# Performance work log

Hardware: AMD Instinct MI355X
Metric: run time of the kernel (lower is better)

The kernel has to match this reference:

```python
import jax, jax.numpy as jnp
import numpy as np

ALPHA_MIN = float(np.exp(-1.0 / 5.0))   # balance=False lower clamp
ALPHA_MAX = float(np.exp(-1.0 / 25.0))  # balance=False upper clamp


@jax.custom_vjp
def spike(u, thr):
    # Heaviside forward: spike if membrane potential exceeds threshold
    return (u > thr).astype(u.dtype)

def _spike_fwd(u, thr):
    return spike(u, thr), (u, thr)

def _spike_bwd(res, g):
    u, thr = res
    # Boxcar surrogate gradient: pass-through within +-0.5 of threshold
    mask = ((u > thr - 0.5) & (u <= thr + 0.5)).astype(g.dtype)
    return (g * mask, jnp.zeros_like(thr))

spike.defvjp(_spike_fwd, _spike_bwd)


def setup_inputs() -> dict:
    key = jax.random.key(0)
    kx, kw, kv, ka = jax.random.split(key, 4)
    B, T, I, H = 32, 1000, 256, 512
    x = jax.random.normal(kx, (B, T, I), dtype=jnp.float32)
    # W ~ U(-sqrt(1/I), sqrt(1/I)) as in nn.init.uniform_
    lim = float(np.sqrt(1.0 / I))
    W = jax.random.uniform(kw, (H, I), minval=-lim, maxval=lim, dtype=jnp.float32)
    # V: orthogonal init
    V = jnp.linalg.qr(jax.random.normal(kv, (H, H), dtype=jnp.float32))[0]
    alpha = jax.random.uniform(ka, (H,), minval=ALPHA_MIN, maxval=ALPHA_MAX, dtype=jnp.float32)
    v_thresh = jnp.ones((H,), dtype=jnp.float32)
    return {"x": x, "W": W, "V": V, "alpha": alpha, "v_thresh": v_thresh}


def reference(x, W, V, alpha, v_thresh):
    # x: [B, T, I]; W: [H, I]; V: [H, H]; alpha, v_thresh: [H]
    a = jnp.clip(alpha, ALPHA_MIN, ALPHA_MAX)
    H = V.shape[0]
    Vz = V * (1.0 - jnp.eye(H, dtype=V.dtype))  # fill_diagonal_(0)
    Wx = jnp.einsum('bti,hi->bth', x, W)        # feedforward drive [B,T,H]

    B = x.shape[0]
    ut0 = jnp.zeros((B, H), dtype=x.dtype)
    st0 = jnp.zeros((B, H), dtype=x.dtype)

    def step(carry, wx_t):
        ut, st = carry
        # leaky integration with recurrent spikes (fix_w_rec=False path)
        ut = a * (ut - st) + (1.0 - a) * (wx_t + st @ Vz)
        st = spike(ut, v_thresh)
        return (ut, st), st

    _, s = jax.lax.scan(step, (ut0, st0), jnp.swapaxes(Wx, 0, 1))  # [T,B,H]
    return jnp.swapaxes(s, 0, 1)  # [B,T,H]
```

## Files before the change

### kernel.cpp

```cpp
#include <hip/hip_runtime.h>

#define BATCH 32
#define TSTEPS 1000
#define KDIM 256
#define HDIM 512
#define NSEG 8
#define SEGL 125
#define SPFD 25

#define ALPHA_MIN_F 0.8187307530779818f
#define ALPHA_MAX_F 0.9607894391523232f

typedef __attribute__((ext_vector_type(8))) short bf16x8;
typedef __attribute__((ext_vector_type(8))) unsigned short u16x8;
typedef __attribute__((ext_vector_type(4))) float f32x4;

static __device__ __forceinline__ unsigned short f2bf(float f) {
  unsigned u = __float_as_uint(f);
  u += 0x7FFF + ((u >> 16) & 1);
  return (unsigned short)(u >> 16);
}
static __device__ __forceinline__ float bf2f(unsigned short s) {
  return __uint_as_float(((unsigned)s) << 16);
}

__global__ void init_fs(int* fs) {
  if (threadIdx.x < BATCH) fs[threadIdx.x] = TSTEPS;
}

__global__ __launch_bounds__(256) void cast_pack(const float* __restrict__ src,
                                                 unsigned short* __restrict__ hi,
                                                 unsigned short* __restrict__ lo,
                                                 int ntiles) {
  const int tile = blockIdx.x * 4 + (threadIdx.x >> 6);
  if (tile >= ntiles) return;
  const int lane = threadIdx.x & 63;
  const int row = tile * 16 + (lane & 15);
  const int kg = lane >> 4;
  const float* sp = src + (size_t)row * KDIM + kg * 8;
  unsigned short* hp = hi + (size_t)tile * 8 * 512 + lane * 8;
  unsigned short* lp = lo + (size_t)tile * 8 * 512 + lane * 8;
#pragma unroll
  for (int ks = 0; ks < 8; ++ks) {
    float4 a = *reinterpret_cast<const float4*>(sp + ks * 32);
    float4 b = *reinterpret_cast<const float4*>(sp + ks * 32 + 4);
    u16x8 h, l;
    h[0] = f2bf(a.x); l[0] = f2bf(a.x - bf2f(h[0]));
    h[1] = f2bf(a.y); l[1] = f2bf(a.y - bf2f(h[1]));
    h[2] = f2bf(a.z); l[2] = f2bf(a.z - bf2f(h[2]));
    h[3] = f2bf(a.w); l[3] = f2bf(a.w - bf2f(h[3]));
    h[4] = f2bf(b.x); l[4] = f2bf(b.x - bf2f(h[4]));
    h[5] = f2bf(b.y); l[5] = f2bf(b.y - bf2f(h[5]));
    h[6] = f2bf(b.z); l[6] = f2bf(b.z - bf2f(h[6]));
    h[7] = f2bf(b.w); l[7] = f2bf(b.w - bf2f(h[7]));
    *reinterpret_cast<u16x8*>(hp + ks * 512) = h;
    *reinterpret_cast<u16x8*>(lp + ks * 512) = l;
  }
}

__global__ __launch_bounds__(128, 2) void gemm_mfma3(
    const float* __restrict__ x, const unsigned short* __restrict__ wph,
    const unsigned short* __restrict__ wpl, float* __restrict__ wx) {
  __shared__ short bsh[2][2][4096];
  const int tid = threadIdx.x;
  const int lane = tid & 63;
  const int wid = tid >> 6;
  const int row = lane & 15;
  const int kg = lane >> 4;
  const int tm = blockIdx.x * 2 + wid;
  const int m0 = tm * 16;

  bf16x8 ah[8], al[8];
  const float* xp = x + (size_t)(m0 + row) * KDIM + kg * 8;
#pragma unroll
  for (int ks = 0; ks < 8; ++ks) {
    float4 f0 = *reinterpret_cast<const float4*>(xp + ks * 32);
    float4 f1 = *reinterpret_cast<const float4*>(xp + ks * 32 + 4);
    bf16x8 hv, lv;
    hv[0] = (short)f2bf(f0.x); lv[0] = (short)f2bf(f0.x - bf2f(hv[0]));
    hv[1] = (short)f2bf(f0.y); lv[1] = (short)f2bf(f0.y - bf2f(hv[1]));
    hv[2] = (short)f2bf(f0.z); lv[2] = (short)f2bf(f0.z - bf2f(hv[2]));
    hv[3] = (short)f2bf(f0.w); lv[3] = (short)f2bf(f0.w - bf2f(hv[3]));
    hv[4] = (short)f2bf(f1.x); lv[4] = (short)f2bf(f1.x - bf2f(hv[4]));
    hv[5] = (short)f2bf(f1.y); lv[5] = (short)f2bf(f1.y - bf2f(hv[5]));
    hv[6] = (short)f2bf(f1.z); lv[6] = (short)f2bf(f1.z - bf2f(hv[6]));
    hv[7] = (short)f2bf(f1.w); lv[7] = (short)f2bf(f1.w - bf2f(hv[7]));
    ah[ks] = hv;
    al[ks] = lv;
  }

#pragma unroll
  for (int r = 0; r < 4; ++r) {
    const int o = r * 1024 + tid * 8;
    *reinterpret_cast<bf16x8*>(&bsh[0][0][o]) =
        *reinterpret_cast<const bf16x8*>(wph + o);
    *reinterpret_cast<bf16x8*>(&bsh[0][1][o]) =
        *reinterpret_cast<const bf16x8*>(wpl + o);
  }
  __syncthreads();

  for (int ct = 0; ct < 32; ++ct) {
    const int buf = ct & 1;
    bf16x8 nh[4], nl[4];
    const bool pre = (ct < 31);
    if (pre) {
      const unsigned short* sh = wph + (size_t)(ct + 1) * 4096;
      const unsigned short* sl = wpl + (size_t)(ct + 1) * 4096;
#pragma unroll
      for (int r = 0; r < 4; ++r) {
        const int o = r * 1024 + tid * 8;
        nh[r] = *reinterpret_cast<const bf16x8*>(sh + o);
        nl[r] = *reinterpret_cast<const bf16x8*>(sl + o);
      }
    }

    f32x4 accA = {0.f, 0.f, 0.f, 0.f};
    f32x4 accB = {0.f, 0.f, 0.f, 0.f};
    f32x4 accC = {0.f, 0.f, 0.f, 0.f};
#pragma unroll
    for (int ks = 0; ks < 8; ++ks) {
      bf16x8 bh = *reinterpret_cast<const bf16x8*>(&bsh[buf][0][ks * 512 + lane * 8]);
      bf16x8 bl = *reinterpret_cast<const bf16x8*>(&bsh[buf][1][ks * 512 + lane * 8]);
      accA = __builtin_amdgcn_mfma_f32_16x16x32_bf16(ah[ks], bh, accA, 0, 0, 0);
      accB = __builtin_amdgcn_mfma_f32_16x16x32_bf16(al[ks], bh, accB, 0, 0, 0);
      accC = __builtin_amdgcn_mfma_f32_16x16x32_bf16(ah[ks], bl, accC, 0, 0, 0);
    }
    const int n0 = ct * 16;
#pragma unroll
    for (int j = 0; j < 4; ++j) {
      wx[(size_t)(m0 + kg * 4 + j) * HDIM + n0 + row] =
          (accA[j] + accB[j]) + accC[j];
    }
    if (pre) {
#pragma unroll
      for (int r = 0; r < 4; ++r) {
        const int o = r * 1024 + tid * 8;
        *reinterpret_cast<bf16x8*>(&bsh[buf ^ 1][0][o]) = nh[r];
        *reinterpret_cast<bf16x8*>(&bsh[buf ^ 1][1][o]) = nl[r];
      }
    }
    __syncthreads();
  }
}

__global__ __launch_bounds__(64) void seg_sum(const float* __restrict__ wx,
                                              const float* __restrict__ alpha,
                                              float* __restrict__ cbuf) {
  const int hb = blockIdx.x & 7;
  const int rest = blockIdx.x >> 3;
  const int seg = rest % 7;
  const int b = rest / 7;
  const int h = (hb << 6) + threadIdx.x;
  const float a = fminf(fmaxf(alpha[h], ALPHA_MIN_F), ALPHA_MAX_F);
  const float na = 1.0f - a;
  const float* wp = wx + ((size_t)b * TSTEPS + seg * SEGL) * HDIM + h;

  float pf[SPFD];
#pragma unroll
  for (int d = 0; d < SPFD; ++d) pf[d] = wp[(size_t)d * HDIM];

  float c = 0.f;
  for (int j0 = 0; j0 < SEGL; j0 += SPFD) {
#pragma unroll
    for (int js = 0; js < SPFD; ++js) {
      const int j = j0 + js;
      const float w = pf[js];
      int jp = j + SPFD;
      if (jp > SEGL - 1) jp = SEGL - 1;
      pf[js] = wp[(size_t)jp * HDIM];
      c = fmaf(a, c, na * w);
    }
  }
  cbuf[(size_t)seg * BATCH * HDIM + (size_t)b * HDIM + h] = c;
}

__global__ __launch_bounds__(64) void seg_scan(const float* __restrict__ wx,
                                               const float* __restrict__ alpha,
                                               const float* __restrict__ vthr,
                                               const float* __restrict__ cbuf,
                                               float* __restrict__ out,
                                               int* __restrict__ fs) {
  const int hb = blockIdx.x & 7;
  const int seg = (blockIdx.x >> 3) & 7;
  const int b = blockIdx.x >> 6;
  const int h = (hb << 6) + threadIdx.x;
  const float a = fminf(fmaxf(alpha[h], ALPHA_MIN_F), ALPHA_MAX_F);
  const float na = 1.0f - a;
  const float th = vthr[h];
  const int t0g = seg * SEGL;
  const float* wp = wx + ((size_t)b * TSTEPS + t0g) * HDIM + h;
  float* op = out + ((size_t)b * TSTEPS + t0g) * HDIM + h;

  float pf[SPFD];
#pragma unroll
  for (int d = 0; d < SPFD; ++d) pf[d] = wp[(size_t)d * HDIM];

  float aL = 1.0f;
  for (int i = 0; i < SEGL; ++i) aL *= a;
  float u = 0.f;
  for (int k = 0; k < seg; ++k)
    u = fmaf(aL, u, cbuf[(size_t)k * BATCH * HDIM + (size_t)b * HDIM + h]);

  float s = 0.f;
  int first = TSTEPS;
  for (int j0 = 0; j0 < SEGL; j0 += SPFD) {
#pragma unroll
    for (int js = 0; js < SPFD; ++js) {
      const int j = j0 + js;
      const float w = pf[js];
      int jp = j + SPFD;
      if (jp > SEGL - 1) jp = SEGL - 1;
      pf[js] = wp[(size_t)jp * HDIM];
      u = fmaf(a, u - s, na * w);
      s = (u > th) ? 1.0f : 0.0f;
      op[(size_t)j * HDIM] = s;
      if (s != 0.0f && first == TSTEPS) {
        first = t0g + j;
        atomicMin(&fs[b], first);
      }
    }
  }
}

static __device__ __forceinline__ void scan_body(const float* wxbuf,
                                                 const float* __restrict__ V,
                                                 const float* __restrict__ alpha,
                                                 const float* __restrict__ vthr,
                                                 float* out, int b) {
  const int l = threadIdx.x;
  const int h0 = 4 * l;
  const int h1 = 256 + 4 * l;

  float4 al0 = *reinterpret_cast<const float4*>(alpha + h0);
  float4 al1 = *reinterpret_cast<const float4*>(alpha + h1);
  float4 th0 = *reinterpret_cast<const float4*>(vthr + h0);
  float4 th1 = *reinterpret_cast<const float4*>(vthr + h1);
  float a[8] = {al0.x, al0.y, al0.z, al0.w, al1.x, al1.y, al1.z, al1.w};
  float th[8] = {th0.x, th0.y, th0.z, th0.w, th1.x, th1.y, th1.z, th1.w};
  float na[8], u[8], s[8], r[8];
#pragma unroll
  for (int j = 0; j < 8; ++j) {
    float c = fminf(fmaxf(a[j], ALPHA_MIN_F), ALPHA_MAX_F);
    a[j] = c; na[j] = 1.0f - c;
    u[j] = 0.f; s[j] = 0.f; r[j] = 0.f;
  }
  const float* wb = wxbuf + (size_t)b * TSTEPS * HDIM;
  float* ob = out + (size_t)b * TSTEPS * HDIM;
  float4 p0[4], p1[4];
#pragma unroll
  for (int d = 0; d < 4; ++d) {
    p0[d] = *reinterpret_cast<const float4*>(wb + (size_t)d * HDIM + h0);
    p1[d] = *reinterpret_cast<const float4*>(wb + (size_t)d * HDIM + h1);
  }
  for (int t0 = 0; t0 < TSTEPS; t0 += 4) {
#pragma unroll
    for (int ts = 0; ts < 4; ++ts) {
      const int t = t0 + ts;
      float w8[8] = {p0[ts].x, p0[ts].y, p0[ts].z, p0[ts].w,
                     p1[ts].x, p1[ts].y, p1[ts].z, p1[ts].w};
      int tpre = t + 4;
      if (tpre > TSTEPS - 1) tpre = TSTEPS - 1;
      p0[ts] = *reinterpret_cast<const float4*>(wb + (size_t)tpre * HDIM + h0);
      p1[ts] = *reinterpret_cast<const float4*>(wb + (size_t)tpre * HDIM + h1);
#pragma unroll
      for (int j = 0; j < 8; ++j) {
        float un = fmaf(a[j], u[j] - s[j], na[j] * (w8[j] + r[j]));
        u[j] = un;
        s[j] = (un > th[j]) ? 1.0f : 0.0f;
      }
      *reinterpret_cast<float4*>(ob + (size_t)t * HDIM + h0) =
          make_float4(s[0], s[1], s[2], s[3]);
      *reinterpret_cast<float4*>(ob + (size_t)t * HDIM + h1) =
          make_float4(s[4], s[5], s[6], s[7]);
      float ssum = s[0] + s[1] + s[2] + s[3] + s[4] + s[5] + s[6] + s[7];
      unsigned long long anym = __ballot(ssum != 0.0f);
      if (anym != 0ull) {
        unsigned long long mk[8];
#pragma unroll
        for (int j = 0; j < 8; ++j) mk[j] = __ballot(s[j] != 0.0f);
        float rr[8] = {0.f, 0.f, 0.f, 0.f, 0.f, 0.f, 0.f, 0.f};
#pragma unroll
        for (int j2 = 0; j2 < 8; ++j2) {
          unsigned long long m = mk[j2];
          while (m) {
            int src = __builtin_ctzll(m);
            m &= m - 1;
            int hin = (j2 < 4) ? (src * 4 + j2) : (256 + src * 4 + (j2 - 4));
            const float* vrow = V + (size_t)hin * HDIM;
            float4 v0 = *reinterpret_cast<const float4*>(vrow + h0);
            float4 v1 = *reinterpret_cast<const float4*>(vrow + h1);
            float vv[8] = {v0.x, v0.y, v0.z, v0.w, v1.x, v1.y, v1.z, v1.w};
#pragma unroll
            for (int j = 0; j < 8; ++j) {
              int hj = (j < 4) ? (h0 + j) : (h1 + j - 4);
              rr[j] += (hj == hin) ? 0.0f : vv[j];
            }
          }
        }
#pragma unroll
        for (int j = 0; j < 8; ++j) r[j] = rr[j];
      } else {
#pragma unroll
        for (int j = 0; j < 8; ++j) r[j] = 0.0f;
      }
    }
  }
}

__global__ __launch_bounds__(64) void fallback_scan(
    const float* wxbuf, const float* __restrict__ V,
    const float* __restrict__ alpha, const float* __restrict__ vthr,
    float* out, const int* __restrict__ fs) {
  const int b = blockIdx.x;
  if (fs[b] >= TSTEPS - 1) return;
  scan_body(wxbuf, V, alpha, vthr, out, b);
}

__global__ __launch_bounds__(64) void rlif_scan(const float* wxbuf,
                                                const float* __restrict__ V,
                                                const float* __restrict__ alpha,
                                                const float* __restrict__ vthr,
                                                float* out) {
  scan_body(wxbuf, V, alpha, vthr, out, blockIdx.x);
}

__global__ __launch_bounds__(256) void gemm_xwT(const float* __restrict__ x,
                                                const float* __restrict__ W,
                                                float* __restrict__ wx) {
  __shared__ float As[32][64];
  __shared__ float Bs[32][64];
  const int m0 = blockIdx.x * 64;
  const int n0 = blockIdx.y * 64;
  const int tid = threadIdx.x;
  const int tx = tid & 15;
  const int ty = tid >> 4;
  const int lr = tid >> 2;
  const int lk = (tid & 3) * 8;

  float acc[4][4] = {};
  for (int k0 = 0; k0 < KDIM; k0 += 32) {
    const float4* ap =
        reinterpret_cast<const float4*>(x + (size_t)(m0 + lr) * KDIM + k0 + lk);
    const float4* bp =
        reinterpret_cast<const float4*>(W + (size_t)(n0 + lr) * KDIM + k0 + lk);
    float4 a0 = ap[0], a1 = ap[1];
    float4 b0 = bp[0], b1 = bp[1];
    __syncthreads();
    As[lk + 0][lr] = a0.x; As[lk + 1][lr] = a0.y;
    As[lk + 2][lr] = a0.z; As[lk + 3][lr] = a0.w;
    As[lk + 4][lr] = a1.x; As[lk + 5][lr] = a1.y;
    As[lk + 6][lr] = a1.z; As[lk + 7][lr] = a1.w;
    Bs[lk + 0][lr] = b0.x; Bs[lk + 1][lr] = b0.y;
    Bs[lk + 2][lr] = b0.z; Bs[lk + 3][lr] = b0.w;
    Bs[lk + 4][lr] = b1.x; Bs[lk + 5][lr] = b1.y;
    Bs[lk + 6][lr] = b1.z; Bs[lk + 7][lr] = b1.w;
    __syncthreads();
#pragma unroll
    for (int k = 0; k < 32; ++k) {
      float4 av = *reinterpret_cast<const float4*>(&As[k][ty * 4]);
      float4 bv = *reinterpret_cast<const float4*>(&Bs[k][tx * 4]);
      float am[4] = {av.x, av.y, av.z, av.w};
      float bn[4] = {bv.x, bv.y, bv.z, bv.w};
#pragma unroll
      for (int i = 0; i < 4; ++i)
#pragma unroll
        for (int j = 0; j < 4; ++j) acc[i][j] = fmaf(am[i], bn[j], acc[i][j]);
    }
  }
#pragma unroll
  for (int i = 0; i < 4; ++i) {
    float4 o = make_float4(acc[i][0], acc[i][1], acc[i][2], acc[i][3]);
    *reinterpret_cast<float4*>(wx + (size_t)(m0 + ty * 4 + i) * HDIM + n0 +
                               tx * 4) = o;
  }
}

extern "C" void kernel_launch(void* const* d_in, const int* in_sizes, int n_in,
                              void* d_out, int out_size, void* d_ws,
                              size_t ws_size, hipStream_t stream) {
  const float* x = (const float*)d_in[0];
  const float* W = (const float*)d_in[1];
  const float* V = (const float*)d_in[2];
  const float* alpha = (const float*)d_in[3];
  const float* vthr = (const float*)d_in[4];
  float* out = (float*)d_out;

  const size_t wx_b = (size_t)BATCH * TSTEPS * HDIM * 4;
  const size_t wh_b = (size_t)HDIM * KDIM * 2;
  const size_t cb_b = (size_t)NSEG * BATCH * HDIM * 4;
  const size_t needA = wx_b + 2 * wh_b + cb_b + 128;
  const size_t needB = wx_b + cb_b + 128;

  char* ws = (char*)d_ws;
  if (ws_size >= needA) {
    float* wx = (float*)ws;
    unsigned short* wph = (unsigned short*)(ws + wx_b);
    unsigned short* wpl = wph + (size_t)HDIM * KDIM;
    float* cbuf = (float*)(ws + wx_b + 2 * wh_b);
    int* fs = (int*)(ws + wx_b + 2 * wh_b + cb_b);

    hipLaunchKernelGGL(init_fs, dim3(1), dim3(64), 0, stream, fs);
    hipLaunchKernelGGL(cast_pack, dim3(8), dim3(256), 0, stream, W, wph, wpl,
                       HDIM / 16);
    hipLaunchKernelGGL(gemm_mfma3, dim3(BATCH * TSTEPS / 32), dim3(128), 0,
                       stream, x, wph, wpl, wx);
    hipLaunchKernelGGL(seg_sum, dim3(BATCH * 7 * 8), dim3(64), 0, stream,
                       wx, alpha, cbuf);
    hipLaunchKernelGGL(seg_scan, dim3(BATCH * NSEG * 8), dim3(64), 0, stream,
                       wx, alpha, vthr, cbuf, out, fs);
    hipLaunchKernelGGL(fallback_scan, dim3(BATCH), dim3(64), 0, stream, wx, V,
                       alpha, vthr, out, fs);
  } else if (ws_size >= needB) {
    float* wx = (float*)ws;
    float* cbuf = (float*)(ws + wx_b);
    int* fs = (int*)(ws + wx_b + cb_b);
    hipLaunchKernelGGL(init_fs, dim3(1), dim3(64), 0, stream, fs);
    hipLaunchKernelGGL(gemm_xwT, dim3(BATCH * TSTEPS / 64, HDIM / 64),
                       dim3(256), 0, stream, x, W, wx);
    hipLaunchKernelGGL(seg_sum, dim3(BATCH * 7 * 8), dim3(64), 0, stream,
                       wx, alpha, cbuf);
    hipLaunchKernelGGL(seg_scan, dim3(BATCH * NSEG * 8), dim3(64), 0, stream,
                       wx, alpha, vthr, cbuf, out, fs);
    hipLaunchKernelGGL(fallback_scan, dim3(BATCH), dim3(64), 0, stream, wx, V,
                       alpha, vthr, out, fs);
  } else {
    float* wx = (ws_size >= wx_b) ? (float*)ws : out;
    hipLaunchKernelGGL(gemm_xwT, dim3(BATCH * TSTEPS / 64, HDIM / 64),
                       dim3(256), 0, stream, x, W, wx);
    hipLaunchKernelGGL(rlif_scan, dim3(BATCH), dim3(64), 0, stream, wx, V,
                       alpha, vthr, out);
  }
}
```

Baseline: 82.65 us.

## Compute two M-tiles per wave in split-bf16 GEMM and fold fs init into cast kernel

Each wave in the MFMA GEMM now processes two 16-row M tiles, so every B fragment read from shared memory is reused twice and the grid is halved. Separately, the fs initialisation moves into the weight cast kernel, removing one kernel launch. The larger tile doubles the A-fragment and accumulator registers per wave, which can lower occupancy, and halving the block count reduces parallelism across CUs.

```diff
diff --git a/kernel.cpp b/kernel.cpp
--- a/kernel.cpp
+++ b/kernel.cpp
@@ -28,10 +28,10 @@
   if (threadIdx.x < BATCH) fs[threadIdx.x] = TSTEPS;
 }
 
-__global__ __launch_bounds__(256) void cast_pack(const float* __restrict__ src,
-                                                 unsigned short* __restrict__ hi,
-                                                 unsigned short* __restrict__ lo,
-                                                 int ntiles) {
+__global__ __launch_bounds__(256) void cast_pack_fs(
+    const float* __restrict__ src, unsigned short* __restrict__ hi,
+    unsigned short* __restrict__ lo, int ntiles, int* __restrict__ fs) {
+  if (blockIdx.x == 0 && threadIdx.x < BATCH) fs[threadIdx.x] = TSTEPS;
   const int tile = blockIdx.x * 4 + (threadIdx.x >> 6);
   if (tile >= ntiles) return;
   const int lane = threadIdx.x & 63;
@@ -58,7 +58,7 @@
   }
 }
 
-__global__ __launch_bounds__(128, 2) void gemm_mfma3(
+__global__ __launch_bounds__(128, 2) void gemm_mfma7(
     const float* __restrict__ x, const unsigned short* __restrict__ wph,
     const unsigned short* __restrict__ wpl, float* __restrict__ wx) {
   __shared__ short bsh[2][2][4096];
@@ -67,26 +67,28 @@
   const int wid = tid >> 6;
   const int row = lane & 15;
   const int kg = lane >> 4;
-  const int tm = blockIdx.x * 2 + wid;
-  const int m0 = tm * 16;
-
-  bf16x8 ah[8], al[8];
-  const float* xp = x + (size_t)(m0 + row) * KDIM + kg * 8;
-#pragma unroll
-  for (int ks = 0; ks < 8; ++ks) {
-    float4 f0 = *reinterpret_cast<const float4*>(xp + ks * 32);
-    float4 f1 = *reinterpret_cast<const float4*>(xp + ks * 32 + 4);
-    bf16x8 hv, lv;
-    hv[0] = (short)f2bf(f0.x); lv[0] = (short)f2bf(f0.x - bf2f(hv[0]));
-    hv[1] = (short)f2bf(f0.y); lv[1] = (short)f2bf(f0.y - bf2f(hv[1]));
-    hv[2] = (short)f2bf(f0.z); lv[2] = (short)f2bf(f0.z - bf2f(hv[2]));
-    hv[3] = (short)f2bf(f0.w); lv[3] = (short)f2bf(f0.w - bf2f(hv[3]));
-    hv[4] = (short)f2bf(f1.x); lv[4] = (short)f2bf(f1.x - bf2f(hv[4]));
-    hv[5] = (short)f2bf(f1.y); lv[5] = (short)f2bf(f1.y - bf2f(hv[5]));
-    hv[6] = (short)f2bf(f1.z); lv[6] = (short)f2bf(f1.z - bf2f(hv[6]));
-    hv[7] = (short)f2bf(f1.w); lv[7] = (short)f2bf(f1.w - bf2f(hv[7]));
-    ah[ks] = hv;
-    al[ks] = lv;
+  const int tmb = (blockIdx.x * 2 + wid) * 2;
+
+  bf16x8 ah[2][8], al[2][8];
+#pragma unroll
+  for (int mt = 0; mt < 2; ++mt) {
+    const float* xp = x + (size_t)((tmb + mt) * 16 + row) * KDIM + kg * 8;
+#pragma unroll
+    for (int ks = 0; ks < 8; ++ks) {
+      float4 f0 = *reinterpret_cast<const float4*>(xp + ks * 32);
+      float4 f1 = *reinterpret_cast<const float4*>(xp + ks * 32 + 4);
+      bf16x8 hv, lv;
+      hv[0] = (short)f2bf(f0.x); lv[0] = (short)f2bf(f0.x - bf2f(hv[0]));
+      hv[1] = (short)f2bf(f0.y); lv[1] = (short)f2bf(f0.y - bf2f(hv[1]));
+      hv[2] = (short)f2bf(f0.z); lv[2] = (short)f2bf(f0.z - bf2f(hv[2]));
+      hv[3] = (short)f2bf(f0.w); lv[3] = (short)f2bf(f0.w - bf2f(hv[3]));
+      hv[4] = (short)f2bf(f1.x); lv[4] = (short)f2bf(f1.x - bf2f(hv[4]));
+      hv[5] = (short)f2bf(f1.y); lv[5] = (short)f2bf(f1.y - bf2f(hv[5]));
+      hv[6] = (short)f2bf(f1.z); lv[6] = (short)f2bf(f1.z - bf2f(hv[6]));
+      hv[7] = (short)f2bf(f1.w); lv[7] = (short)f2bf(f1.w - bf2f(hv[7]));
+      ah[mt][ks] = hv;
+      al[mt][ks] = lv;
+    }
   }
 
 #pragma unroll
@@ -114,22 +116,29 @@
       }
     }
 
-    f32x4 accA = {0.f, 0.f, 0.f, 0.f};
-    f32x4 accB = {0.f, 0.f, 0.f, 0.f};
-    f32x4 accC = {0.f, 0.f, 0.f, 0.f};
+    f32x4 accA[2] = {{0.f, 0.f, 0.f, 0.f}, {0.f, 0.f, 0.f, 0.f}};
+    f32x4 accB[2] = {{0.f, 0.f, 0.f, 0.f}, {0.f, 0.f, 0.f, 0.f}};
+    f32x4 accC[2] = {{0.f, 0.f, 0.f, 0.f}, {0.f, 0.f, 0.f, 0.f}};
 #pragma unroll
     for (int ks = 0; ks < 8; ++ks) {
       bf16x8 bh = *reinterpret_cast<const bf16x8*>(&bsh[buf][0][ks * 512 + lane * 8]);
       bf16x8 bl = *reinterpret_cast<const bf16x8*>(&bsh[buf][1][ks * 512 + lane * 8]);
-      accA = __builtin_amdgcn_mfma_f32_16x16x32_bf16(ah[ks], bh, accA, 0, 0, 0);
-      accB = __builtin_amdgcn_mfma_f32_16x16x32_bf16(al[ks], bh, accB, 0, 0, 0);
-      accC = __builtin_amdgcn_mfma_f32_16x16x32_bf16(ah[ks], bl, accC, 0, 0, 0);
+#pragma unroll
+      for (int mt = 0; mt < 2; ++mt) {
+        accA[mt] = __builtin_amdgcn_mfma_f32_16x16x32_bf16(ah[mt][ks], bh, accA[mt], 0, 0, 0);
+        accB[mt] = __builtin_amdgcn_mfma_f32_16x16x32_bf16(al[mt][ks], bh, accB[mt], 0, 0, 0);
+        accC[mt] = __builtin_amdgcn_mfma_f32_16x16x32_bf16(ah[mt][ks], bl, accC[mt], 0, 0, 0);
+      }
     }
     const int n0 = ct * 16;
 #pragma unroll
-    for (int j = 0; j < 4; ++j) {
-      wx[(size_t)(m0 + kg * 4 + j) * HDIM + n0 + row] =
-          (accA[j] + accB[j]) + accC[j];
+    for (int mt = 0; mt < 2; ++mt) {
+      const int m0 = (tmb + mt) * 16;
+#pragma unroll
+      for (int j = 0; j < 4; ++j) {
+        wx[(size_t)(m0 + kg * 4 + j) * HDIM + n0 + row] =
+            (accA[mt][j] + accB[mt][j]) + accC[mt][j];
+      }
     }
     if (pre) {
 #pragma unroll
@@ -399,10 +408,9 @@
     float* cbuf = (float*)(ws + wx_b + 2 * wh_b);
     int* fs = (int*)(ws + wx_b + 2 * wh_b + cb_b);
 
-    hipLaunchKernelGGL(init_fs, dim3(1), dim3(64), 0, stream, fs);
-    hipLaunchKernelGGL(cast_pack, dim3(8), dim3(256), 0, stream, W, wph, wpl,
-                       HDIM / 16);
-    hipLaunchKernelGGL(gemm_mfma3, dim3(BATCH * TSTEPS / 32), dim3(128), 0,
+    hipLaunchKernelGGL(cast_pack_fs, dim3(8), dim3(256), 0, stream, W, wph,
+                       wpl, HDIM / 16, fs);
+    hipLaunchKernelGGL(gemm_mfma7, dim3(BATCH * TSTEPS / 64), dim3(128), 0,
                        stream, x, wph, wpl, wx);
     hipLaunchKernelGGL(seg_sum, dim3(BATCH * 7 * 8), dim3(64), 0, stream,
                        wx, alpha, cbuf);
```

Measured after the change: 88.76 us. 7.4% more time.

## Fuse segment sum and segment scan into one cooperative kernel with grid sync

Applied to the files above, without the earlier changes.

Replaces the separate seg_sum and seg_scan kernels with a single cooperative kernel. Each block loads its 125-step segment of wx into registers once, computes the segment carry, waits at a grid-wide sync, then runs the spike scan from the register copy. This removes the second read of wx from global memory and one kernel launch. init_fs is also folded into cast_pack to drop another launch. The trade-offs are a 125-float register array per thread, which may spill, and the requirement that all 2048 blocks be co-resident for the grid sync.

```diff
diff --git a/kernel.cpp b/kernel.cpp
--- a/kernel.cpp
+++ b/kernel.cpp
@@ -1,4 +1,7 @@
 #include <hip/hip_runtime.h>
+#include <hip/hip_cooperative_groups.h>
+
+namespace cg = cooperative_groups;
 
 #define BATCH 32
 #define TSTEPS 1000
@@ -28,10 +31,10 @@
   if (threadIdx.x < BATCH) fs[threadIdx.x] = TSTEPS;
 }
 
-__global__ __launch_bounds__(256) void cast_pack(const float* __restrict__ src,
-                                                 unsigned short* __restrict__ hi,
-                                                 unsigned short* __restrict__ lo,
-                                                 int ntiles) {
+__global__ __launch_bounds__(256) void cast_pack_fs(
+    const float* __restrict__ src, unsigned short* __restrict__ hi,
+    unsigned short* __restrict__ lo, int ntiles, int* __restrict__ fs) {
+  if (blockIdx.x == 0 && threadIdx.x < BATCH) fs[threadIdx.x] = TSTEPS;
   const int tile = blockIdx.x * 4 + (threadIdx.x >> 6);
   if (tile >= ntiles) return;
   const int lane = threadIdx.x & 63;
@@ -141,6 +144,155 @@
     }
     __syncthreads();
   }
+}
+
+__global__ __launch_bounds__(64, 2) void seg_fused(
+    const float* __restrict__ wx, const float* __restrict__ alpha,
+    const float* __restrict__ vthr, float* __restrict__ cbuf,
+    float* __restrict__ out, int* __restrict__ fs) {
+  const int hb = blockIdx.x & 7;
+  const int seg = (blockIdx.x >> 3) & 7;
+  const int b = blockIdx.x >> 6;
+  const int h = (hb << 6) + threadIdx.x;
+  const float a = fminf(fmaxf(alpha[h], ALPHA_MIN_F), ALPHA_MAX_F);
+  const float na = 1.0f - a;
+  const int t0g = seg * SEGL;
+  const float* wp = wx + ((size_t)b * TSTEPS + t0g) * HDIM + h;
+
+  float w[SEGL];
+#pragma unroll
+  for (int j = 0; j < SEGL; ++j) w[j] = wp[(size_t)j * HDIM];
+
+  float c = 0.f;
+#pragma unroll
+  for (int j = 0; j < SEGL; ++j) c = fmaf(a, c, na * w[j]);
+  if (seg < NSEG - 1)
+    cbuf[(size_t)seg * BATCH * HDIM + (size_t)b * HDIM + h] = c;
+
+  cg::this_grid().sync();
+
+  float aL = 1.0f;
+  for (int i = 0; i < SEGL; ++i) aL *= a;
+  float u = 0.f;
+  for (int k = 0; k < seg; ++k)
+    u = fmaf(aL, u, cbuf[(size_t)k * BATCH * HDIM + (size_t)b * HDIM + h]);
+
+  const float th = vthr[h];
+  float* op = out + ((size_t)b * TSTEPS + t0g) * HDIM + h;
+  float s = 0.f;
+  int first = TSTEPS;
+#pragma unroll
+  for (int j = 0; j < SEGL; ++j) {
+    u = fmaf(a, u - s, na * w[j]);
+    s = (u > th) ? 1.0f : 0.0f;
+    op[(size_t)j * HDIM] = s;
+    if (s != 0.0f && first == TSTEPS) {
+      first = t0g + j;
+      atomicMin(&fs[b], first);
+    }
+  }
+}
+
+static __device__ __forceinline__ void scan_body(const float* wxbuf,
+                                                 const float* __restrict__ V,
+                                                 const float* __restrict__ alpha,
+                                                 const float* __restrict__ vthr,
+                                                 float* out, int b) {
+  const int l = threadIdx.x;
+  const int h0 = 4 * l;
+  const int h1 = 256 + 4 * l;
+
+  float4 al0 = *reinterpret_cast<const float4*>(alpha + h0);
+  float4 al1 = *reinterpret_cast<const float4*>(alpha + h1);
+  float4 th0 = *reinterpret_cast<const float4*>(vthr + h0);
+  float4 th1 = *reinterpret_cast<const float4*>(vthr + h1);
+  float a[8] = {al0.x, al0.y, al0.z, al0.w, al1.x, al1.y, al1.z, al1.w};
+  float th[8] = {th0.x, th0.y, th0.z, th0.w, th1.x, th1.y, th1.z, th1.w};
+  float na[8], u[8], s[8], r[8];
+#pragma unroll
+  for (int j = 0; j < 8; ++j) {
+    float c = fminf(fmaxf(a[j], ALPHA_MIN_F), ALPHA_MAX_F);
+    a[j] = c; na[j] = 1.0f - c;
+    u[j] = 0.f; s[j] = 0.f; r[j] = 0.f;
+  }
+  const float* wb = wxbuf + (size_t)b * TSTEPS * HDIM;
+  float* ob = out + (size_t)b * TSTEPS * HDIM;
+  float4 p0[4], p1[4];
+#pragma unroll
+  for (int d = 0; d < 4; ++d) {
+    p0[d] = *reinterpret_cast<const float4*>(wb + (size_t)d * HDIM + h0);
+    p1[d] = *reinterpret_cast<const float4*>(wb + (size_t)d * HDIM + h1);
+  }
+  for (int t0 = 0; t0 < TSTEPS; t0 += 4) {
+#pragma unroll
+    for (int ts = 0; ts < 4; ++ts) {
+      const int t = t0 + ts;
+      float w8[8] = {p0[ts].x, p0[ts].y, p0[ts].z, p0[ts].w,
+                     p1[ts].x, p1[ts].y, p1[ts].z, p1[ts].w};
+      int tpre = t + 4;
+      if (tpre > TSTEPS - 1) tpre = TSTEPS - 1;
+      p0[ts] = *reinterpret_cast<const float4*>(wb + (size_t)tpre * HDIM + h0);
+      p1[ts] = *reinterpret_cast<const float4*>(wb + (size_t)tpre * HDIM + h1);
+#pragma unroll
+      for (int j = 0; j < 8; ++j) {
+        float un = fmaf(a[j], u[j] - s[j], na[j] * (w8[j] + r[j]));
+        u[j] = un;
+        s[j] = (un > th[j]) ? 1.0f : 0.0f;
+      }
+      *reinterpret_cast<float4*>(ob + (size_t)t * HDIM + h0) =
+          make_float4(s[0], s[1], s[2], s[3]);
+      *reinterpret_cast<float4*>(ob + (size_t)t * HDIM + h1) =
+          make_float4(s[4], s[5], s[6], s[7]);
+      float ssum = s[0] + s[1] + s[2] + s[3] + s[4] + s[5] + s[6] + s[7];
+      unsigned long long anym = __ballot(ssum != 0.0f);
+      if (anym != 0ull) {
+        unsigned long long mk[8];
+#pragma unroll
+        for (int j = 0; j < 8; ++j) mk[j] = __ballot(s[j] != 0.0f);
+        float rr[8] = {0.f, 0.f, 0.f, 0.f, 0.f, 0.f, 0.f, 0.f};
+#pragma unroll
+        for (int j2 = 0; j2 < 8; ++j2) {
+          unsigned long long m = mk[j2];
+          while (m) {
+            int src = __builtin_ctzll(m);
+            m &= m - 1;
+            int hin = (j2 < 4) ? (src * 4 + j2) : (256 + src * 4 + (j2 - 4));
+            const float* vrow = V + (size_t)hin * HDIM;
+            float4 v0 = *reinterpret_cast<const float4*>(vrow + h0);
+            float4 v1 = *reinterpret_cast<const float4*>(vrow + h1);
+            float vv[8] = {v0.x, v0.y, v0.z, v0.w, v1.x, v1.y, v1.z, v1.w};
+#pragma unroll
+            for (int j = 0; j < 8; ++j) {
+              int hj = (j < 4) ? (h0 + j) : (h1 + j - 4);
+              rr[j] += (hj == hin) ? 0.0f : vv[j];
+            }
+          }
+        }
+#pragma unroll
+        for (int j = 0; j < 8; ++j) r[j] = rr[j];
+      } else {
+#pragma unroll
+        for (int j = 0; j < 8; ++j) r[j] = 0.0f;
+      }
+    }
+  }
+}
+
+__global__ __launch_bounds__(64) void fallback_scan(
+    const float* wxbuf, const float* __restrict__ V,
+    const float* __restrict__ alpha, const float* __restrict__ vthr,
+    float* out, const int* __restrict__ fs) {
+  const int b = blockIdx.x;
+  if (fs[b] >= TSTEPS - 1) return;
+  scan_body(wxbuf, V, alpha, vthr, out, b);
+}
+
+__global__ __launch_bounds__(64) void rlif_scan(const float* wxbuf,
+                                                const float* __restrict__ V,
+                                                const float* __restrict__ alpha,
+                                                const float* __restrict__ vthr,
+                                                float* out) {
+  scan_body(wxbuf, V, alpha, vthr, out, blockIdx.x);
 }
 
 __global__ __launch_bounds__(64) void seg_sum(const float* __restrict__ wx,
@@ -220,108 +372,6 @@
       }
     }
   }
-}
-
-static __device__ __forceinline__ void scan_body(const float* wxbuf,
-                                                 const float* __restrict__ V,
-                                                 const float* __restrict__ alpha,
-                                                 const float* __restrict__ vthr,
-                                                 float* out, int b) {
-  const int l = threadIdx.x;
-  const int h0 = 4 * l;
-  const int h1 = 256 + 4 * l;
-
-  float4 al0 = *reinterpret_cast<const float4*>(alpha + h0);
-  float4 al1 = *reinterpret_cast<const float4*>(alpha + h1);
-  float4 th0 = *reinterpret_cast<const float4*>(vthr + h0);
-  float4 th1 = *reinterpret_cast<const float4*>(vthr + h1);
-  float a[8] = {al0.x, al0.y, al0.z, al0.w, al1.x, al1.y, al1.z, al1.w};
-  float th[8] = {th0.x, th0.y, th0.z, th0.w, th1.x, th1.y, th1.z, th1.w};
-  float na[8], u[8], s[8], r[8];
-#pragma unroll
-  for (int j = 0; j < 8; ++j) {
-    float c = fminf(fmaxf(a[j], ALPHA_MIN_F), ALPHA_MAX_F);
-    a[j] = c; na[j] = 1.0f - c;
-    u[j] = 0.f; s[j] = 0.f; r[j] = 0.f;
-  }
-  const float* wb = wxbuf + (size_t)b * TSTEPS * HDIM;
-  float* ob = out + (size_t)b * TSTEPS * HDIM;
-  float4 p0[4], p1[4];
-#pragma unroll
-  for (int d = 0; d < 4; ++d) {
-    p0[d] = *reinterpret_cast<const float4*>(wb + (size_t)d * HDIM + h0);
-    p1[d] = *reinterpret_cast<const float4*>(wb + (size_t)d * HDIM + h1);
-  }
-  for (int t0 = 0; t0 < TSTEPS; t0 += 4) {
-#pragma unroll
-    for (int ts = 0; ts < 4; ++ts) {
-      const int t = t0 + ts;
-      float w8[8] = {p0[ts].x, p0[ts].y, p0[ts].z, p0[ts].w,
-                     p1[ts].x, p1[ts].y, p1[ts].z, p1[ts].w};
-      int tpre = t + 4;
-      if (tpre > TSTEPS - 1) tpre = TSTEPS - 1;
-      p0[ts] = *reinterpret_cast<const float4*>(wb + (size_t)tpre * HDIM + h0);
-      p1[ts] = *reinterpret_cast<const float4*>(wb + (size_t)tpre * HDIM + h1);
-#pragma unroll
-      for (int j = 0; j < 8; ++j) {
-        float un = fmaf(a[j], u[j] - s[j], na[j] * (w8[j] + r[j]));
-        u[j] = un;
-        s[j] = (un > th[j]) ? 1.0f : 0.0f;
-      }
-      *reinterpret_cast<float4*>(ob + (size_t)t * HDIM + h0) =
-          make_float4(s[0], s[1], s[2], s[3]);
-      *reinterpret_cast<float4*>(ob + (size_t)t * HDIM + h1) =
-          make_float4(s[4], s[5], s[6], s[7]);
-      float ssum = s[0] + s[1] + s[2] + s[3] + s[4] + s[5] + s[6] + s[7];
-      unsigned long long anym = __ballot(ssum != 0.0f);
-      if (anym != 0ull) {
-        unsigned long long mk[8];
-#pragma unroll
-        for (int j = 0; j < 8; ++j) mk[j] = __ballot(s[j] != 0.0f);
-        float rr[8] = {0.f, 0.f, 0.f, 0.f, 0.f, 0.f, 0.f, 0.f};
-#pragma unroll
-        for (int j2 = 0; j2 < 8; ++j2) {
-          unsigned long long m = mk[j2];
-          while (m) {
-            int src = __builtin_ctzll(m);
-            m &= m - 1;
-            int hin = (j2 < 4) ? (src * 4 + j2) : (256 + src * 4 + (j2 - 4));
-            const float* vrow = V + (size_t)hin * HDIM;
-            float4 v0 = *reinterpret_cast<const float4*>(vrow + h0);
-            float4 v1 = *reinterpret_cast<const float4*>(vrow + h1);
-            float vv[8] = {v0.x, v0.y, v0.z, v0.w, v1.x, v1.y, v1.z, v1.w};
-#pragma unroll
-            for (int j = 0; j < 8; ++j) {
-              int hj = (j < 4) ? (h0 + j) : (h1 + j - 4);
-              rr[j] += (hj == hin) ? 0.0f : vv[j];
-            }
-          }
-        }
-#pragma unroll
-        for (int j = 0; j < 8; ++j) r[j] = rr[j];
-      } else {
-#pragma unroll
-        for (int j = 0; j < 8; ++j) r[j] = 0.0f;
-      }
-    }
-  }
-}
-
-__global__ __launch_bounds__(64) void fallback_scan(
-    const float* wxbuf, const float* __restrict__ V,
-    const float* __restrict__ alpha, const float* __restrict__ vthr,
-    float* out, const int* __restrict__ fs) {
-  const int b = blockIdx.x;
-  if (fs[b] >= TSTEPS - 1) return;
-  scan_body(wxbuf, V, alpha, vthr, out, b);
-}
-
-__global__ __launch_bounds__(64) void rlif_scan(const float* wxbuf,
-                                                const float* __restrict__ V,
-                                                const float* __restrict__ alpha,
-                                                const float* __restrict__ vthr,
-                                                float* out) {
-  scan_body(wxbuf, V, alpha, vthr, out, blockIdx.x);
 }
 
 __global__ __launch_bounds__(256) void gemm_xwT(const float* __restrict__ x,
@@ -399,15 +449,18 @@
     float* cbuf = (float*)(ws + wx_b + 2 * wh_b);
     int* fs = (int*)(ws + wx_b + 2 * wh_b + cb_b);
 
-    hipLaunchKernelGGL(init_fs, dim3(1), dim3(64), 0, stream, fs);
-    hipLaunchKernelGGL(cast_pack, dim3(8), dim3(256), 0, stream, W, wph, wpl,
-                       HDIM / 16);
+    hipLaunchKernelGGL(cast_pack_fs, dim3(8), dim3(256), 0, stream, W, wph,
+                       wpl, HDIM / 16, fs);
     hipLaunchKernelGGL(gemm_mfma3, dim3(BATCH * TSTEPS / 32), dim3(128), 0,
                        stream, x, wph, wpl, wx);
-    hipLaunchKernelGGL(seg_sum, dim3(BATCH * 7 * 8), dim3(64), 0, stream,
-                       wx, alpha, cbuf);
-    hipLaunchKernelGGL(seg_scan, dim3(BATCH * NSEG * 8), dim3(64), 0, stream,
-                       wx, alpha, vthr, cbuf, out, fs);
+    {
+      const float* wxc = wx;
+      void* cargs[] = {(void*)&wxc,  (void*)&alpha, (void*)&vthr,
+                       (void*)&cbuf, (void*)&out,   (void*)&fs};
+      hipLaunchCooperativeKernel((const void*)seg_fused,
+                                 dim3(BATCH * NSEG * 8), dim3(64), cargs, 0,
+                                 stream);
+    }
     hipLaunchKernelGGL(fallback_scan, dim3(BATCH), dim3(64), 0, stream, wx, V,
                        alpha, vthr, out, fs);
   } else if (ws_size >= needB) {
```

Result: slower. 236.0 us (+185.6%).
